# Performance work log

Measured on AMD Instinct MI355X. Metric: run time of the kernel, lower is better.

The kernel has to match this reference:

```python
import jax, jax.numpy as jnp
import numpy as np

HIDDEN = 2048
INTER = 5632
NCODES = 4096
VEC = 8
TOKENS = 4096


def dequant(codebook, idx, scale):
    # codebook: [NCODES, VEC]; idx: [out, in//VEC] int32; scale: [out]
    out, ncol = idx.shape
    w = codebook[idx].reshape(out, ncol * VEC)  # [out, in]
    return w * scale[:, None]


def setup_inputs() -> dict:
    key = jax.random.key(0)
    ks = jax.random.split(key, 10)
    return {
        "x": jax.random.normal(ks[0], (TOKENS, HIDDEN), dtype=jnp.float32),
        "codebook_gate": jax.random.normal(ks[1], (NCODES, VEC), dtype=jnp.float32),
        "idx_gate": jax.random.randint(ks[2], (INTER, HIDDEN // VEC), 0, NCODES, dtype=jnp.int32),
        "scale_gate": jax.random.uniform(ks[3], (INTER,), dtype=jnp.float32, minval=0.01, maxval=0.05),
        "codebook_up": jax.random.normal(ks[4], (NCODES, VEC), dtype=jnp.float32),
        "idx_up": jax.random.randint(ks[5], (INTER, HIDDEN // VEC), 0, NCODES, dtype=jnp.int32),
        "scale_up": jax.random.uniform(ks[6], (INTER,), dtype=jnp.float32, minval=0.01, maxval=0.05),
        "codebook_down": jax.random.normal(ks[7], (NCODES, VEC), dtype=jnp.float32),
        "idx_down": jax.random.randint(ks[8], (HIDDEN, INTER // VEC), 0, NCODES, dtype=jnp.int32),
        "scale_down": jax.random.uniform(ks[9], (HIDDEN,), dtype=jnp.float32, minval=0.01, maxval=0.05),
    }


def reference(x, codebook_gate, idx_gate, scale_gate,
              codebook_up, idx_up, scale_up,
              codebook_down, idx_down, scale_down):
    # Dequantize trellis/codebook weights, then SwiGLU:
    # out = down( silu(gate(x)) * up(x) )
    w_gate = dequant(codebook_gate, idx_gate, scale_gate)  # [INTER, HIDDEN]
    w_up = dequant(codebook_up, idx_up, scale_up)          # [INTER, HIDDEN]
    w_down = dequant(codebook_down, idx_down, scale_down)  # [HIDDEN, INTER]
    gate = jax.nn.silu(x @ w_gate.T)                       # [T, INTER]
    up = x @ w_up.T                                        # [T, INTER]
    return (gate * up) @ w_down.T                          # [T, HIDDEN]
```

## Files before the change

kernel.cpp:

```cpp
#include <hip/hip_runtime.h>

#define HIDDEN 2048
#define INTER  5632
#define TOKENS 4096

#define BM 128
#define BN 128
#define BK 64

using bf16x8 = __attribute__((ext_vector_type(8))) __bf16;
using f32x4  = __attribute__((ext_vector_type(4))) float;

__device__ __forceinline__ unsigned short f2bf(float f) {
    unsigned int u = __float_as_uint(f);
    u += 0x7FFFu + ((u >> 16) & 1u);
    return (unsigned short)(u >> 16);
}

__global__ __launch_bounds__(256) void prep_kernel(
        const float* __restrict__ x, unsigned short* __restrict__ xb,
        const int* __restrict__ ig, const float* __restrict__ cbg,
        const float* __restrict__ sg, unsigned short* __restrict__ wg,
        const int* __restrict__ iu, const float* __restrict__ cbu,
        const float* __restrict__ su, unsigned short* __restrict__ wu,
        const int* __restrict__ idn, const float* __restrict__ cbd,
        const float* __restrict__ sd, unsigned short* __restrict__ wd) {
    int b = blockIdx.x;
    if (b < 4096) {
        int t = b * 256 + threadIdx.x;
        const float4* x4 = (const float4*)x;
        float4 a = x4[2 * t];
        float4 c = x4[2 * t + 1];
        uint4 o;
        o.x = f2bf(a.x) | ((unsigned int)f2bf(a.y) << 16);
        o.y = f2bf(a.z) | ((unsigned int)f2bf(a.w) << 16);
        o.z = f2bf(c.x) | ((unsigned int)f2bf(c.y) << 16);
        o.w = f2bf(c.z) | ((unsigned int)f2bf(c.w) << 16);
        ((uint4*)xb)[t] = o;
        return;
    }
    const int* idx; const float* cb; const float* scale; unsigned short* w; int ncol8;
    if (b < 4096 + 5632)      { b -= 4096;         idx = ig;  cb = cbg; scale = sg; w = wg; ncol8 = HIDDEN / 8; }
    else if (b < 4096 + 11264){ b -= 4096 + 5632;  idx = iu;  cb = cbu; scale = su; w = wu; ncol8 = HIDDEN / 8; }
    else                      { b -= 4096 + 11264; idx = idn; cb = cbd; scale = sd; w = wd; ncol8 = INTER / 8; }
    int t = b * 256 + threadIdx.x;
    int row = t / ncol8;
    int id = idx[t];
    float s = scale[row];
    const float4* c4 = (const float4*)(cb + ((size_t)id << 3));
    float4 a = c4[0];
    float4 c = c4[1];
    uint4 o;
    o.x = f2bf(a.x * s) | ((unsigned int)f2bf(a.y * s) << 16);
    o.y = f2bf(a.z * s) | ((unsigned int)f2bf(a.w * s) << 16);
    o.z = f2bf(c.x * s) | ((unsigned int)f2bf(c.y * s) << 16);
    o.w = f2bf(c.z * s) | ((unsigned int)f2bf(c.w * s) << 16);
    ((uint4*)w)[t] = o;
}


__global__ __launch_bounds__(256, 2) void gemm1_kernel(const unsigned short* __restrict__ X,
                                                       const unsigned short* __restrict__ Wg,
                                                       const unsigned short* __restrict__ Wu,
                                                       unsigned short* __restrict__ H) {
    __shared__ unsigned short As[BM * BK];
    __shared__ unsigned short Bgs[BN * BK];
    __shared__ unsigned short Bus[BN * BK];

    const int tid  = threadIdx.x;
    const int lane = tid & 63;
    const int wave = tid >> 6;
    const int m0 = blockIdx.x * BM;
    const int n0 = blockIdx.y * BN;

    const int srow = tid >> 3;
    const int scol = (tid & 7) << 3;
    const int gcol = (((tid & 7) ^ (srow & 7))) << 3;

    const int wr = wave >> 1;
    const int wc = wave & 1;
    const int ln15 = lane & 15;
    const int lq = lane >> 4;
    const int swr = ln15 & 7;

    f32x4 accg[4][4], accu[4][4];
    const f32x4 z = {0.f, 0.f, 0.f, 0.f};
    for (int i = 0; i < 4; ++i)
        for (int j = 0; j < 4; ++j) { accg[i][j] = z; accu[i][j] = z; }

    for (int kt = 0; kt < HIDDEN / BK; ++kt) {
        const int k0 = kt * BK;
        __syncthreads();
#pragma unroll
        for (int i = 0; i < 4; ++i) {
            const int r = i * 32 + srow;
            __builtin_amdgcn_global_load_lds(
                (__attribute__((address_space(1))) void*)(X + (size_t)(m0 + r) * HIDDEN + k0 + gcol),
                (__attribute__((address_space(3))) void*)(As + r * BK + scol), 16, 0, 0);
            __builtin_amdgcn_global_load_lds(
                (__attribute__((address_space(1))) void*)(Wg + (size_t)(n0 + r) * HIDDEN + k0 + gcol),
                (__attribute__((address_space(3))) void*)(Bgs + r * BK + scol), 16, 0, 0);
            __builtin_amdgcn_global_load_lds(
                (__attribute__((address_space(1))) void*)(Wu + (size_t)(n0 + r) * HIDDEN + k0 + gcol),
                (__attribute__((address_space(3))) void*)(Bus + r * BK + scol), 16, 0, 0);
        }
        __syncthreads();
#pragma unroll
        for (int ks = 0; ks < 2; ++ks) {
            bf16x8 af[4], bg[4], bu[4];
            const int pofs = (((ks * 4 + lq) ^ swr)) << 3;
#pragma unroll
            for (int im = 0; im < 4; ++im)
                af[im] = *(const bf16x8*)(As + (wr * 64 + im * 16 + ln15) * BK + pofs);
#pragma unroll
            for (int in = 0; in < 4; ++in) {
                bg[in] = *(const bf16x8*)(Bgs + (wc * 64 + in * 16 + ln15) * BK + pofs);
                bu[in] = *(const bf16x8*)(Bus + (wc * 64 + in * 16 + ln15) * BK + pofs);
            }
#pragma unroll
            for (int im = 0; im < 4; ++im)
#pragma unroll
                for (int in = 0; in < 4; ++in) {
                    accg[im][in] = __builtin_amdgcn_mfma_f32_16x16x32_bf16(af[im], bg[in], accg[im][in], 0, 0, 0);
                    accu[im][in] = __builtin_amdgcn_mfma_f32_16x16x32_bf16(af[im], bu[in], accu[im][in], 0, 0, 0);
                }
        }
    }

#pragma unroll
    for (int im = 0; im < 4; ++im)
#pragma unroll
        for (int in = 0; in < 4; ++in) {
            const int row = m0 + wr * 64 + im * 16 + lq * 4;
            const int col = n0 + wc * 64 + in * 16 + ln15;
#pragma unroll
            for (int r = 0; r < 4; ++r) {
                float g = accg[im][in][r];
                float u = accu[im][in][r];
                float h = g * (1.0f / (1.0f + __expf(-g))) * u;
                H[(size_t)(row + r) * INTER + col] = f2bf(h);
            }
        }
}

__global__ __launch_bounds__(256, 2) void gemm2_kernel(const unsigned short* __restrict__ Hin,
                                                       const unsigned short* __restrict__ Wd,
                                                       float* __restrict__ Out) {
    __shared__ unsigned short As[BM * BK];
    __shared__ unsigned short Bs[BN * BK];

    const int tid  = threadIdx.x;
    const int lane = tid & 63;
    const int wave = tid >> 6;
    const int m0 = blockIdx.x * BM;
    const int n0 = blockIdx.y * BN;

    const int srow = tid >> 3;
    const int scol = (tid & 7) << 3;
    const int gcol = (((tid & 7) ^ (srow & 7))) << 3;

    const int wr = wave >> 1;
    const int wc = wave & 1;
    const int ln15 = lane & 15;
    const int lq = lane >> 4;
    const int swr = ln15 & 7;

    f32x4 acc[4][4];
    const f32x4 z = {0.f, 0.f, 0.f, 0.f};
    for (int i = 0; i < 4; ++i)
        for (int j = 0; j < 4; ++j) acc[i][j] = z;

    for (int kt = 0; kt < INTER / BK; ++kt) {
        const int k0 = kt * BK;
        __syncthreads();
#pragma unroll
        for (int i = 0; i < 4; ++i) {
            const int r = i * 32 + srow;
            __builtin_amdgcn_global_load_lds(
                (__attribute__((address_space(1))) void*)(Hin + (size_t)(m0 + r) * INTER + k0 + gcol),
                (__attribute__((address_space(3))) void*)(As + r * BK + scol), 16, 0, 0);
            __builtin_amdgcn_global_load_lds(
                (__attribute__((address_space(1))) void*)(Wd + (size_t)(n0 + r) * INTER + k0 + gcol),
                (__attribute__((address_space(3))) void*)(Bs + r * BK + scol), 16, 0, 0);
        }
        __syncthreads();
#pragma unroll
        for (int ks = 0; ks < 2; ++ks) {
            bf16x8 af[4], bf[4];
            const int pofs = (((ks * 4 + lq) ^ swr)) << 3;
#pragma unroll
            for (int im = 0; im < 4; ++im)
                af[im] = *(const bf16x8*)(As + (wr * 64 + im * 16 + ln15) * BK + pofs);
#pragma unroll
            for (int in = 0; in < 4; ++in)
                bf[in] = *(const bf16x8*)(Bs + (wc * 64 + in * 16 + ln15) * BK + pofs);
#pragma unroll
            for (int im = 0; im < 4; ++im)
#pragma unroll
                for (int in = 0; in < 4; ++in)
                    acc[im][in] = __builtin_amdgcn_mfma_f32_16x16x32_bf16(af[im], bf[in], acc[im][in], 0, 0, 0);
        }
    }

#pragma unroll
    for (int im = 0; im < 4; ++im)
#pragma unroll
        for (int in = 0; in < 4; ++in) {
            const int row = m0 + wr * 64 + im * 16 + lq * 4;
            const int col = n0 + wc * 64 + in * 16 + ln15;
#pragma unroll
            for (int r = 0; r < 4; ++r)
                Out[(size_t)(row + r) * HIDDEN + col] = acc[im][in][r];
        }
}

extern "C" void kernel_launch(void* const* d_in, const int* in_sizes, int n_in,
                              void* d_out, int out_size, void* d_ws, size_t ws_size,
                              hipStream_t stream) {
    (void)in_sizes; (void)n_in; (void)out_size; (void)ws_size;

    const float* x   = (const float*)d_in[0];
    const float* cbg = (const float*)d_in[1];
    const int*   ig  = (const int*)d_in[2];
    const float* sg  = (const float*)d_in[3];
    const float* cbu = (const float*)d_in[4];
    const int*   iu  = (const int*)d_in[5];
    const float* su  = (const float*)d_in[6];
    const float* cbd = (const float*)d_in[7];
    const int*   idn = (const int*)d_in[8];
    const float* sd  = (const float*)d_in[9];
    float* out = (float*)d_out;

    char* p = (char*)d_ws;
    unsigned short* Xb = (unsigned short*)p; p += (size_t)TOKENS * HIDDEN * 2;
    unsigned short* Wg = (unsigned short*)p; p += (size_t)INTER * HIDDEN * 2;
    unsigned short* Wu = (unsigned short*)p; p += (size_t)INTER * HIDDEN * 2;
    unsigned short* Wd = (unsigned short*)p; p += (size_t)HIDDEN * INTER * 2;
    unsigned short* H  = (unsigned short*)p; p += (size_t)TOKENS * INTER * 2;

    prep_kernel<<<dim3(4096 + 3 * 5632), dim3(256), 0, stream>>>(
        x, Xb, ig, cbg, sg, Wg, iu, cbu, su, Wu, idn, cbd, sd, Wd);

    gemm1_kernel<<<dim3(TOKENS / BM, INTER / BN), dim3(256), 0, stream>>>(Xb, Wg, Wu, H);
    gemm2_kernel<<<dim3(TOKENS / BM, HIDDEN / BN), dim3(256), 0, stream>>>(H, Wd, out);
}
```

Before: 394.7 us.

## Double-buffer LDS tiles with halved BK to overlap global loads with MFMA

Both GEMM kernels now keep two LDS buffers with BK reduced to 32, so total shared memory per block stays the same. Each iteration issues the async global-to-LDS copies for the next K tile before running MFMAs on the current tile, with one barrier per iteration instead of two. The XOR swizzle is rewritten for the narrower 32-element rows. The goal is to hide global load latency behind compute. The risks are twice as many loop iterations, each with less MFMA work to cover the barrier, and that the compiler may insert conservative waits on the async copies, which would cancel the overlap.

```diff
diff --git a/kernel.cpp b/kernel.cpp
--- a/kernel.cpp
+++ b/kernel.cpp
@@ -6,7 +6,7 @@
 
 #define BM 128
 #define BN 128
-#define BK 64
+#define BK 32
 
 using bf16x8 = __attribute__((ext_vector_type(8))) __bf16;
 using f32x4  = __attribute__((ext_vector_type(4))) float;
@@ -16,6 +16,10 @@
     u += 0x7FFFu + ((u >> 16) & 1u);
     return (unsigned short)(u >> 16);
 }
+
+#define GLDS(gptr, lptr) \
+    __builtin_amdgcn_global_load_lds((__attribute__((address_space(1))) void*)(gptr), \
+                                     (__attribute__((address_space(3))) void*)(lptr), 16, 0, 0)
 
 __global__ __launch_bounds__(256) void prep_kernel(
         const float* __restrict__ x, unsigned short* __restrict__ xb,
@@ -63,9 +67,9 @@
                                                        const unsigned short* __restrict__ Wg,
                                                        const unsigned short* __restrict__ Wu,
                                                        unsigned short* __restrict__ H) {
-    __shared__ unsigned short As[BM * BK];
-    __shared__ unsigned short Bgs[BN * BK];
-    __shared__ unsigned short Bus[BN * BK];
+    __shared__ unsigned short As[2 * BM * BK];
+    __shared__ unsigned short Bgs[2 * BN * BK];
+    __shared__ unsigned short Bus[2 * BN * BK];
 
     const int tid  = threadIdx.x;
     const int lane = tid & 63;
@@ -73,58 +77,68 @@
     const int m0 = blockIdx.x * BM;
     const int n0 = blockIdx.y * BN;
 
-    const int srow = tid >> 3;
-    const int scol = (tid & 7) << 3;
-    const int gcol = (((tid & 7) ^ (srow & 7))) << 3;
+    const int srow = tid >> 2;
+    const int scol = (tid & 3) << 3;
+    const int gcol = (((tid & 3) ^ ((srow >> 1) & 3))) << 3;
 
     const int wr = wave >> 1;
     const int wc = wave & 1;
     const int ln15 = lane & 15;
     const int lq = lane >> 4;
-    const int swr = ln15 & 7;
+    const int pofs = ((lq ^ ((ln15 >> 1) & 3))) << 3;
+
+    const size_t gA0 = (size_t)(m0 + srow) * HIDDEN + gcol;
+    const size_t gB0 = (size_t)(n0 + srow) * HIDDEN + gcol;
+    const int ldsOfs = srow * BK + scol;
 
     f32x4 accg[4][4], accu[4][4];
     const f32x4 z = {0.f, 0.f, 0.f, 0.f};
     for (int i = 0; i < 4; ++i)
         for (int j = 0; j < 4; ++j) { accg[i][j] = z; accu[i][j] = z; }
 
-    for (int kt = 0; kt < HIDDEN / BK; ++kt) {
-        const int k0 = kt * BK;
+    const int NT = HIDDEN / BK;
+
+    {
+        GLDS(X  + gA0,            As  + ldsOfs);
+        GLDS(X  + gA0 + 64*HIDDEN, As  + ldsOfs + 64*BK);
+        GLDS(Wg + gB0,            Bgs + ldsOfs);
+        GLDS(Wg + gB0 + 64*HIDDEN, Bgs + ldsOfs + 64*BK);
+        GLDS(Wu + gB0,            Bus + ldsOfs);
+        GLDS(Wu + gB0 + 64*HIDDEN, Bus + ldsOfs + 64*BK);
+    }
+
+    for (int kt = 0; kt < NT; ++kt) {
         __syncthreads();
-#pragma unroll
-        for (int i = 0; i < 4; ++i) {
-            const int r = i * 32 + srow;
-            __builtin_amdgcn_global_load_lds(
-                (__attribute__((address_space(1))) void*)(X + (size_t)(m0 + r) * HIDDEN + k0 + gcol),
-                (__attribute__((address_space(3))) void*)(As + r * BK + scol), 16, 0, 0);
-            __builtin_amdgcn_global_load_lds(
-                (__attribute__((address_space(1))) void*)(Wg + (size_t)(n0 + r) * HIDDEN + k0 + gcol),
-                (__attribute__((address_space(3))) void*)(Bgs + r * BK + scol), 16, 0, 0);
-            __builtin_amdgcn_global_load_lds(
-                (__attribute__((address_space(1))) void*)(Wu + (size_t)(n0 + r) * HIDDEN + k0 + gcol),
-                (__attribute__((address_space(3))) void*)(Bus + r * BK + scol), 16, 0, 0);
-        }
-        __syncthreads();
-#pragma unroll
-        for (int ks = 0; ks < 2; ++ks) {
-            bf16x8 af[4], bg[4], bu[4];
-            const int pofs = (((ks * 4 + lq) ^ swr)) << 3;
-#pragma unroll
-            for (int im = 0; im < 4; ++im)
-                af[im] = *(const bf16x8*)(As + (wr * 64 + im * 16 + ln15) * BK + pofs);
+        if (kt + 1 < NT) {
+            const int nb = (kt + 1) & 1;
+            const size_t k1 = (size_t)(kt + 1) * BK;
+            GLDS(X  + gA0 + k1,             As  + nb*BM*BK + ldsOfs);
+            GLDS(X  + gA0 + k1 + 64*HIDDEN, As  + nb*BM*BK + ldsOfs + 64*BK);
+            GLDS(Wg + gB0 + k1,             Bgs + nb*BN*BK + ldsOfs);
+            GLDS(Wg + gB0 + k1 + 64*HIDDEN, Bgs + nb*BN*BK + ldsOfs + 64*BK);
+            GLDS(Wu + gB0 + k1,             Bus + nb*BN*BK + ldsOfs);
+            GLDS(Wu + gB0 + k1 + 64*HIDDEN, Bus + nb*BN*BK + ldsOfs + 64*BK);
+        }
+        const unsigned short* Ab = As  + (kt & 1) * BM * BK;
+        const unsigned short* Gb = Bgs + (kt & 1) * BN * BK;
+        const unsigned short* Ub = Bus + (kt & 1) * BN * BK;
+
+        bf16x8 af[4], bg[4], bu[4];
+#pragma unroll
+        for (int im = 0; im < 4; ++im)
+            af[im] = *(const bf16x8*)(Ab + (wr * 64 + im * 16 + ln15) * BK + pofs);
+#pragma unroll
+        for (int in = 0; in < 4; ++in) {
+            bg[in] = *(const bf16x8*)(Gb + (wc * 64 + in * 16 + ln15) * BK + pofs);
+            bu[in] = *(const bf16x8*)(Ub + (wc * 64 + in * 16 + ln15) * BK + pofs);
+        }
+#pragma unroll
+        for (int im = 0; im < 4; ++im)
 #pragma unroll
             for (int in = 0; in < 4; ++in) {
-                bg[in] = *(const bf16x8*)(Bgs + (wc * 64 + in * 16 + ln15) * BK + pofs);
-                bu[in] = *(const bf16x8*)(Bus + (wc * 64 + in * 16 + ln15) * BK + pofs);
+                accg[im][in] = __builtin_amdgcn_mfma_f32_16x16x32_bf16(af[im], bg[in], accg[im][in], 0, 0, 0);
+                accu[im][in] = __builtin_amdgcn_mfma_f32_16x16x32_bf16(af[im], bu[in], accu[im][in], 0, 0, 0);
             }
-#pragma unroll
-            for (int im = 0; im < 4; ++im)
-#pragma unroll
-                for (int in = 0; in < 4; ++in) {
-                    accg[im][in] = __builtin_amdgcn_mfma_f32_16x16x32_bf16(af[im], bg[in], accg[im][in], 0, 0, 0);
-                    accu[im][in] = __builtin_amdgcn_mfma_f32_16x16x32_bf16(af[im], bu[in], accu[im][in], 0, 0, 0);
-                }
-        }
     }
 
 #pragma unroll
@@ -146,8 +160,8 @@
 __global__ __launch_bounds__(256, 2) void gemm2_kernel(const unsigned short* __restrict__ Hin,
                                                        const unsigned short* __restrict__ Wd,
                                                        float* __restrict__ Out) {
-    __shared__ unsigned short As[BM * BK];
-    __shared__ unsigned short Bs[BN * BK];
+    __shared__ unsigned short As[2 * BM * BK];
+    __shared__ unsigned short Bs[2 * BN * BK];
 
     const int tid  = threadIdx.x;
     const int lane = tid & 63;
@@ -155,51 +169,59 @@
     const int m0 = blockIdx.x * BM;
     const int n0 = blockIdx.y * BN;
 
-    const int srow = tid >> 3;
-    const int scol = (tid & 7) << 3;
-    const int gcol = (((tid & 7) ^ (srow & 7))) << 3;
+    const int srow = tid >> 2;
+    const int scol = (tid & 3) << 3;
+    const int gcol = (((tid & 3) ^ ((srow >> 1) & 3))) << 3;
 
     const int wr = wave >> 1;
     const int wc = wave & 1;
     const int ln15 = lane & 15;
     const int lq = lane >> 4;
-    const int swr = ln15 & 7;
+    const int pofs = ((lq ^ ((ln15 >> 1) & 3))) << 3;
+
+    const size_t gA0 = (size_t)(m0 + srow) * INTER + gcol;
+    const size_t gB0 = (size_t)(n0 + srow) * INTER + gcol;
+    const int ldsOfs = srow * BK + scol;
 
     f32x4 acc[4][4];
     const f32x4 z = {0.f, 0.f, 0.f, 0.f};
     for (int i = 0; i < 4; ++i)
         for (int j = 0; j < 4; ++j) acc[i][j] = z;
 
-    for (int kt = 0; kt < INTER / BK; ++kt) {
-        const int k0 = kt * BK;
+    const int NT = INTER / BK;
+
+    {
+        GLDS(Hin + gA0,            As + ldsOfs);
+        GLDS(Hin + gA0 + 64*INTER, As + ldsOfs + 64*BK);
+        GLDS(Wd  + gB0,            Bs + ldsOfs);
+        GLDS(Wd  + gB0 + 64*INTER, Bs + ldsOfs + 64*BK);
+    }
+
+    for (int kt = 0; kt < NT; ++kt) {
         __syncthreads();
-#pragma unroll
-        for (int i = 0; i < 4; ++i) {
-            const int r = i * 32 + srow;
-            __builtin_amdgcn_global_load_lds(
-                (__attribute__((address_space(1))) void*)(Hin + (size_t)(m0 + r) * INTER + k0 + gcol),
-                (__attribute__((address_space(3))) void*)(As + r * BK + scol), 16, 0, 0);
-            __builtin_amdgcn_global_load_lds(
-                (__attribute__((address_space(1))) void*)(Wd + (size_t)(n0 + r) * INTER + k0 + gcol),
-                (__attribute__((address_space(3))) void*)(Bs + r * BK + scol), 16, 0, 0);
-        }
-        __syncthreads();
-#pragma unroll
-        for (int ks = 0; ks < 2; ++ks) {
-            bf16x8 af[4], bf[4];
-            const int pofs = (((ks * 4 + lq) ^ swr)) << 3;
-#pragma unroll
-            for (int im = 0; im < 4; ++im)
-                af[im] = *(const bf16x8*)(As + (wr * 64 + im * 16 + ln15) * BK + pofs);
+        if (kt + 1 < NT) {
+            const int nb = (kt + 1) & 1;
+            const size_t k1 = (size_t)(kt + 1) * BK;
+            GLDS(Hin + gA0 + k1,            As + nb*BM*BK + ldsOfs);
+            GLDS(Hin + gA0 + k1 + 64*INTER, As + nb*BM*BK + ldsOfs + 64*BK);
+            GLDS(Wd  + gB0 + k1,            Bs + nb*BN*BK + ldsOfs);
+            GLDS(Wd  + gB0 + k1 + 64*INTER, Bs + nb*BN*BK + ldsOfs + 64*BK);
+        }
+        const unsigned short* Ab = As + (kt & 1) * BM * BK;
+        const unsigned short* Bb = Bs + (kt & 1) * BN * BK;
+
+        bf16x8 af[4], bf[4];
+#pragma unroll
+        for (int im = 0; im < 4; ++im)
+            af[im] = *(const bf16x8*)(Ab + (wr * 64 + im * 16 + ln15) * BK + pofs);
+#pragma unroll
+        for (int in = 0; in < 4; ++in)
+            bf[in] = *(const bf16x8*)(Bb + (wc * 64 + in * 16 + ln15) * BK + pofs);
+#pragma unroll
+        for (int im = 0; im < 4; ++im)
 #pragma unroll
             for (int in = 0; in < 4; ++in)
-                bf[in] = *(const bf16x8*)(Bs + (wc * 64 + in * 16 + ln15) * BK + pofs);
-#pragma unroll
-            for (int im = 0; im < 4; ++im)
-#pragma unroll
-                for (int in = 0; in < 4; ++in)
-                    acc[im][in] = __builtin_amdgcn_mfma_f32_16x16x32_bf16(af[im], bf[in], acc[im][in], 0, 0, 0);
-        }
+                acc[im][in] = __builtin_amdgcn_mfma_f32_16x16x32_bf16(af[im], bf[in], acc[im][in], 0, 0, 0);
     }
 
 #pragma unroll
```

New measurement: 492.8 us. 1.25x slower.
